# Kernel tuning notes

Hardware: AMD Instinct MI355X
Metric: run time of the kernel (lower is better)

## Reference

```python
import jax, jax.numpy as jnp
import numpy as np

DIM = 1024
HEADS = 32
HEAD_DIM = DIM // HEADS
SR_RATIO = 2
N_RATIO = SR_RATIO * SR_RATIO  # AvgPool1d kernel/stride
BN_EPS = 1e-6


def setup_inputs() -> dict:
    key = jax.random.key(0)
    ks = jax.random.split(key, 10)
    B, N, C = 4, 2048, DIM
    s = C ** -0.5
    return {
        "x": jax.random.normal(ks[0], (B, N, C), dtype=jnp.float32),
        # torch.nn.Linear weights, shape [out, in]; applied as x @ W.T
        "Wq": jax.random.normal(ks[1], (C, C), dtype=jnp.float32) * s,
        "Wk": jax.random.normal(ks[2], (C, C), dtype=jnp.float32) * s,
        "Wv": jax.random.normal(ks[3], (C, C), dtype=jnp.float32) * s,
        "Wp": jax.random.normal(ks[4], (C, C), dtype=jnp.float32) * s,
        "bp": jax.random.normal(ks[5], (C,), dtype=jnp.float32) * 0.01,
        # BatchNorm1d (eval mode) affine + running stats over channel dim C
        "bn_gamma": jnp.ones((C,), dtype=jnp.float32),
        "bn_beta": jnp.zeros((C,), dtype=jnp.float32),
        "bn_mean": jax.random.normal(ks[6], (C,), dtype=jnp.float32) * 0.01,
        "bn_var": jnp.ones((C,), dtype=jnp.float32) + jax.random.uniform(ks[7], (C,), dtype=jnp.float32) * 0.1,
    }


def reference(x, Wq, Wk, Wv, Wp, bp, bn_gamma, bn_beta, bn_mean, bn_var):
    B, N, C = x.shape
    scale = HEAD_DIM ** -0.5
    # Q from full-resolution tokens
    q = (x @ Wq.T).reshape(B, N, HEADS, HEAD_DIM).transpose(0, 2, 1, 3)  # [B,H,N,d]
    # spatial reduction: AvgPool1d(kernel=N_RATIO, stride=N_RATIO) over tokens
    xr = x.reshape(B, N // N_RATIO, N_RATIO, C).mean(axis=2)  # [B,M,C]
    # BatchNorm1d eval: normalize channel dim with running stats
    xr = (xr - bn_mean) * jax.lax.rsqrt(bn_var + BN_EPS) * bn_gamma + bn_beta
    M = xr.shape[1]
    k = (xr @ Wk.T).reshape(B, M, HEADS, HEAD_DIM).transpose(0, 2, 1, 3)  # [B,H,M,d]
    v = (xr @ Wv.T).reshape(B, M, HEADS, HEAD_DIM).transpose(0, 2, 1, 3)  # [B,H,M,d]
    # NOTE: no softmax in the original module — raw scaled scores feed the second matmul
    attn = jnp.einsum("bhnd,bhmd->bhnm", q, k) * scale  # [B,H,N,M]
    out = jnp.einsum("bhnm,bhmd->bhnd", attn, v)        # [B,H,N,d]
    out = out.transpose(0, 2, 1, 3).reshape(B, N, C)
    return out @ Wp.T + bp
```

## Files before the change

### kernel.cpp

```cpp
#include <hip/hip_runtime.h>
#include <stdint.h>

#define DEVFN __device__ __forceinline__

typedef __attribute__((ext_vector_type(8))) short s16x8;
typedef __attribute__((ext_vector_type(4))) float f32x4;

DEVFN float bf2f(uint16_t u) {
  union { uint32_t i; float f; } v; v.i = ((uint32_t)u) << 16; return v.f;
}
DEVFN uint16_t f2bf(float f) {
  union { float f; uint32_t i; } v; v.f = f;
  uint32_t u = v.i;
  return (uint16_t)((u + 0x7FFFu + ((u >> 16) & 1u)) >> 16);
}

DEVFN void gload_lds16(const void* g, void* l) {
  __builtin_amdgcn_global_load_lds(
      (const __attribute__((address_space(1))) uint32_t*)g,
      (__attribute__((address_space(3))) uint32_t*)l, 16, 0, 0);
}

__global__ __launch_bounds__(256)
void prep_kernel(const float* __restrict__ x,
                 const float* __restrict__ bn_g, const float* __restrict__ bn_b,
                 const float* __restrict__ bn_m, const float* __restrict__ bn_v,
                 const float* __restrict__ Wk, const float* __restrict__ Wv,
                 const float* __restrict__ Wp,
                 uint16_t* __restrict__ Xh,
                 uint16_t* __restrict__ XRh,
                 uint16_t* __restrict__ Wkvh,
                 uint16_t* __restrict__ Wph)
{
  const int t = threadIdx.x;
  const int bid = blockIdx.x;
  if (bid < 2048) {
    const int prow = bid;
    const int c0 = t * 4;
    const size_t xbase = (size_t)prow * 4096 + c0;
    float s[4] = {0.f, 0.f, 0.f, 0.f};
#pragma unroll
    for (int r = 0; r < 4; ++r) {
      const float4 w = *(const float4*)(x + xbase + (size_t)r * 1024);
      const float vv[4] = { w.x, w.y, w.z, w.w };
      uint64_t wh = 0;
#pragma unroll
      for (int j = 0; j < 4; ++j) {
        wh |= ((uint64_t)f2bf(vv[j])) << (16 * j);
        s[j] += vv[j];
      }
      *(uint64_t*)(Xh + xbase + (size_t)r * 1024) = wh;
    }
    uint64_t wh = 0;
#pragma unroll
    for (int j = 0; j < 4; ++j) {
      const int c = c0 + j;
      const float y = (s[j] * 0.25f - bn_m[c]) / sqrtf(bn_v[c] + 1e-6f) * bn_g[c] + bn_b[c];
      wh |= ((uint64_t)f2bf(y)) << (16 * j);
    }
    *(uint64_t*)(XRh + (size_t)prow * 1024 + c0) = wh;
  } else {
    const int wb = bid - 2048;
    const int which = wb >> 10;
    const int i = (wb & 1023) * 256 + t;
    const float* src = (which == 0) ? Wk : (which == 1) ? Wv : Wp;
    const float4 v = ((const float4*)src)[i];
    const float vv[4] = { v.x, v.y, v.z, v.w };
    uint64_t wh = 0;
#pragma unroll
    for (int j = 0; j < 4; ++j)
      wh |= ((uint64_t)f2bf(vv[j])) << (16 * j);
    if (which == 2) {
      ((uint64_t*)Wph)[i] = wh;
    } else {
      ((uint64_t*)Wkvh)[(size_t)which * (1024 * 1024 / 4) + i] = wh;
    }
  }
}

template<bool BATCHB, bool AMODA, int EPI, bool KSPLIT2, bool SMALLM>
__global__ __launch_bounds__(256, 2)
void gemm_nt(const uint16_t* __restrict__ A0,
             const uint16_t* __restrict__ B0,
             float* __restrict__ C32, uint16_t* __restrict__ Cb0,
             const float* __restrict__ bias,
             int M, int N, int K, int rows_per_batch)
{
  constexpr int BM = SMALLM ? 64 : 128, BN = 128, BK = 128;
  constexpr int WCN = SMALLM ? 4 : 2;
  constexpr int WNW = BN / WCN;
  constexpr int NREP = WNW / 16;
  constexpr int APASS = SMALLM ? 4 : 8;
  constexpr int BPASS = 8;
  __shared__ uint16_t sA[BM * BK];
  __shared__ uint16_t sB[BN * BK];

  const int t = threadIdx.x;
  const int lane = t & 63;
  const int wave = t >> 6;
  const int wr = wave / WCN, wc = wave % WCN;
  const int fq = lane >> 4, fr = lane & 15;

  const int nwg = gridDim.x;
  const int cpx = nwg >> 3;
  const int orig = blockIdx.x;
  const int swz = (orig & 7) * cpx + (orig >> 3);
  const int nbx = N >> 7;
  const int bm = (swz / nbx) * BM;
  const int bn = (swz % nbx) * BN;

  const uint16_t* Ap = A0;
  const uint16_t* Bp = B0;
  if (BATCHB)
    Bp += (size_t)(bm / rows_per_batch) * (size_t)N * (size_t)K;
  if (KSPLIT2) {
    const size_t half = (size_t)blockIdx.y * M * N;
    if (EPI == 1) Cb0 += half; else C32 += half;
  }

  f32x4 acc[4][NREP];
#pragma unroll
  for (int m = 0; m < 4; ++m)
#pragma unroll
    for (int n = 0; n < NREP; ++n) acc[m][n] = (f32x4)0.0f;

  auto STAGE = [&](int kt) {
#pragma unroll
    for (int i = 0; i < APASS; ++i) {
      const int X = t * 16 + i * 4096;
      const int r = X >> 8;
      const int g = ((X >> 4) & 15) ^ (r & 7);
      const int kcol = (kt << 7) + g * 8;
      const int arow = AMODA ? ((bm + r) & 1023) : (bm + r);
      gload_lds16(Ap + (size_t)arow * K + kcol, (char*)(&sA[0]) + X);
    }
#pragma unroll
    for (int i = 0; i < BPASS; ++i) {
      const int X = t * 16 + i * 4096;
      const int r = X >> 8;
      const int g = ((X >> 4) & 15) ^ (r & 7);
      const int kcol = (kt << 7) + g * 8;
      gload_lds16(Bp + (size_t)(bn + r) * K + kcol, (char*)(&sB[0]) + X);
    }
  };

  const int nkt = K >> (KSPLIT2 ? 8 : 7);
  const int kt0 = KSPLIT2 ? (blockIdx.y * nkt) : 0;
  const int ktend = kt0 + nkt;

  STAGE(kt0);
  for (int kt = kt0; kt < ktend; ++kt) {
    __syncthreads();

    s16x8 av[4][4], bv[4][NREP];
#pragma unroll
    for (int ks = 0; ks < 4; ++ks) {
#pragma unroll
      for (int m = 0; m < 4; ++m) {
        const int ra = wr * 64 + m * 16 + fr;
        const int offA = ra * 256 + ((((ks << 2) + fq) ^ (ra & 7)) << 4);
        av[ks][m] = *(const s16x8*)((const char*)(&sA[0]) + offA);
      }
#pragma unroll
      for (int n = 0; n < NREP; ++n) {
        const int rb = wc * WNW + n * 16 + fr;
        const int offB = rb * 256 + ((((ks << 2) + fq) ^ (rb & 7)) << 4);
        bv[ks][n] = *(const s16x8*)((const char*)(&sB[0]) + offB);
      }
    }

    __syncthreads();
    if (kt + 1 < ktend) STAGE(kt + 1);

#pragma unroll
    for (int ks = 0; ks < 4; ++ks)
#pragma unroll
      for (int m = 0; m < 4; ++m)
#pragma unroll
        for (int n = 0; n < NREP; ++n)
          acc[m][n] = __builtin_amdgcn_mfma_f32_16x16x32_bf16(
              av[ks][m], bv[ks][n], acc[m][n], 0, 0, 0);
  }

#pragma unroll
  for (int m = 0; m < 4; ++m) {
#pragma unroll
    for (int n = 0; n < NREP; ++n) {
#pragma unroll
      for (int j = 0; j < 4; ++j) {
        const int row = bm + wr * 64 + m * 16 + fq * 4 + j;
        const int col = bn + wc * WNW + n * 16 + fr;
        const size_t idx = (size_t)row * N + col;
        float v = acc[m][n][j];
        if constexpr (EPI == 0) {
          C32[idx] = v;
        } else if constexpr (EPI == 1) {
          Cb0[idx] = f2bf(v);
        } else {
          C32[idx] = v + bias[col];
        }
      }
    }
  }
}

__global__ __launch_bounds__(256)
void kv1_kernel(const uint16_t* __restrict__ KVcat, float* __restrict__ part)
{
  const int bid = blockIdx.x;
  const int bh = bid >> 3, ch = bid & 7;
  const int b = bh >> 5, h = bh & 31;
  const int t = threadIdx.x;
  __shared__ float sK[64][32];
  __shared__ float sV[64][32];
  const int f = t >> 3, e0 = (t & 7) * 4;
  const int lr = t >> 2, q = t & 3;
  const size_t rowb = (size_t)(b * 512 + ch * 64 + lr) * 2048 + h * 32 + q * 8;
  const size_t H = (size_t)2048 * 2048;
  const s16x8 k0 = *(const s16x8*)(KVcat + rowb);
  const s16x8 k1 = *(const s16x8*)(KVcat + H + rowb);
  const s16x8 v0 = *(const s16x8*)(KVcat + rowb + 1024);
  const s16x8 v1 = *(const s16x8*)(KVcat + H + rowb + 1024);
#pragma unroll
  for (int j = 0; j < 8; ++j) {
    sK[lr][q * 8 + j] = bf2f((uint16_t)k0[j]) + bf2f((uint16_t)k1[j]);
    sV[lr][q * 8 + j] = bf2f((uint16_t)v0[j]) + bf2f((uint16_t)v1[j]);
  }
  __syncthreads();
  float a0 = 0.f, a1 = 0.f, a2 = 0.f, a3 = 0.f;
#pragma unroll 16
  for (int mm = 0; mm < 64; ++mm) {
    const float kf = sK[mm][f];
    const float4 vv = *(const float4*)&sV[mm][e0];
    a0 += kf * vv.x; a1 += kf * vv.y; a2 += kf * vv.z; a3 += kf * vv.w;
  }
  float* o = part + ((size_t)bid * 32 + f) * 32 + e0;
  o[0] = a0; o[1] = a1; o[2] = a2; o[3] = a3;
}

__global__ __launch_bounds__(256)
void t_kernel(const float* __restrict__ part, const float* __restrict__ Wq,
              uint16_t* __restrict__ Tth)
{
  const int bid = blockIdx.x;
  const int b = bid >> 7, h = (bid >> 2) & 31, cc = bid & 3;
  const int bh = b * 32 + h;
  const int t = threadIdx.x;
  __shared__ float sKV[32][32];
  {
    const int f = t >> 3, e0 = (t & 7) * 4;
    f32x4 a = (f32x4)0.0f;
#pragma unroll
    for (int ch = 0; ch < 8; ++ch)
      a += *(const f32x4*)(part + ((size_t)(bh * 8 + ch) * 32 + f) * 32 + e0);
    a *= 0.17677669529663687f;
    *(f32x4*)&sKV[f][e0] = a;
  }
  __syncthreads();
  const int c = cc * 256 + t;
  f32x4 acc[8];
#pragma unroll
  for (int i = 0; i < 8; ++i) acc[i] = (f32x4)0.0f;
  const float* wqp = Wq + (size_t)(h * 32) * 1024 + c;
#pragma unroll 8
  for (int f = 0; f < 32; ++f) {
    const float wq = wqp[(size_t)f * 1024];
#pragma unroll
    for (int i = 0; i < 8; ++i) {
      const f32x4 kv = *(const f32x4*)&sKV[f][i * 4];
      acc[i] += kv * wq;
    }
  }
  const size_t o = (((size_t)b << 10) + c) * 1024 + h * 32;
#pragma unroll
  for (int i = 0; i < 8; ++i) {
    uint64_t wh = 0;
#pragma unroll
    for (int j = 0; j < 4; ++j)
      wh |= ((uint64_t)f2bf(acc[i][j])) << (16 * j);
    *(uint64_t*)(Tth + o + i * 4) = wh;
  }
}

extern "C" void kernel_launch(void* const* d_in, const int* in_sizes, int n_in,
                              void* d_out, int out_size, void* d_ws, size_t ws_size,
                              hipStream_t stream)
{
  const float* x   = (const float*)d_in[0];
  const float* Wq  = (const float*)d_in[1];
  const float* Wk  = (const float*)d_in[2];
  const float* Wv  = (const float*)d_in[3];
  const float* Wp  = (const float*)d_in[4];
  const float* bp  = (const float*)d_in[5];
  const float* bng = (const float*)d_in[6];
  const float* bnb = (const float*)d_in[7];
  const float* bnm = (const float*)d_in[8];
  const float* bnv = (const float*)d_in[9];
  float* out = (float*)d_out;

  char* ws = (char*)d_ws;
  size_t off = 0;
  auto alloc = [&](size_t bytes) {
    char* p = ws + off;
    off += (bytes + 255) & ~(size_t)255;
    return p;
  };
  uint16_t* Xh   = (uint16_t*)alloc((size_t)8192 * 1024 * 2);
  uint16_t* XRh  = (uint16_t*)alloc((size_t)2048 * 1024 * 2);
  uint16_t* Wkvh = (uint16_t*)alloc((size_t)2048 * 1024 * 2);
  uint16_t* Wph  = (uint16_t*)alloc((size_t)1024 * 1024 * 2);
  uint16_t* KVcat= (uint16_t*)alloc((size_t)2 * 2048 * 2048 * 2);
  uint16_t* Gh   = (uint16_t*)alloc((size_t)4096 * 1024 * 2);
  uint16_t* Tth = KVcat;
  float* KVpart = (float*)Gh;

  prep_kernel<<<5120, 256, 0, stream>>>(x, bng, bnb, bnm, bnv, Wk, Wv, Wp,
                                        Xh, XRh, Wkvh, Wph);
  gemm_nt<false, false, 1, true, false><<<dim3(256, 2), 256, 0, stream>>>(
      XRh, Wkvh, nullptr, KVcat, nullptr,
      2048, 2048, 1024, 1 << 30);
  kv1_kernel<<<1024, 256, 0, stream>>>(KVcat, KVpart);
  t_kernel<<<512, 256, 0, stream>>>(KVpart, Wq, Tth);
  gemm_nt<true, true, 1, false, true><<<512, 256, 0, stream>>>(
      Wph, Tth, nullptr, Gh, nullptr,
      4096, 1024, 1024, 1024);
  gemm_nt<true, false, 2, false, false><<<512, 256, 0, stream>>>(
      Xh, Gh, out, nullptr, bp,
      8192, 1024, 1024, 2048);
}
```

Baseline: 85.47 us.

## Switch GEMM to 32x32x16 MFMA and drop register-prefetch overlap

Replaces the 16x16x32 bf16 MFMA tiling with 32x32x16 MFMA instructions, reorganizing the per-wave accumulators, LDS fragment reads and the epilogue index mapping. The main loop is also restructured: the prior scheme loaded all LDS fragments into registers, then issued the next tile's global->LDS copy before computing. Now each iteration stages, syncs, then reads and computes per k-slice. Larger MFMA tiles cut LDS reads per flop and register pressure. The cost is that global loads no longer overlap with MFMA work.

```diff
diff --git a/kernel.cpp b/kernel.cpp
--- a/kernel.cpp
+++ b/kernel.cpp
@@ -5,6 +5,7 @@
 
 typedef __attribute__((ext_vector_type(8))) short s16x8;
 typedef __attribute__((ext_vector_type(4))) float f32x4;
+typedef __attribute__((ext_vector_type(16))) float f32x16;
 
 DEVFN float bf2f(uint16_t u) {
   union { uint32_t i; float f; } v; v.i = ((uint32_t)u) << 16; return v.f;
@@ -89,7 +90,8 @@
   constexpr int BM = SMALLM ? 64 : 128, BN = 128, BK = 128;
   constexpr int WCN = SMALLM ? 4 : 2;
   constexpr int WNW = BN / WCN;
-  constexpr int NREP = WNW / 16;
+  constexpr int NT = WNW / 32;
+  constexpr int MT = 2;
   constexpr int APASS = SMALLM ? 4 : 8;
   constexpr int BPASS = 8;
   __shared__ uint16_t sA[BM * BK];
@@ -99,7 +101,8 @@
   const int lane = t & 63;
   const int wave = t >> 6;
   const int wr = wave / WCN, wc = wave % WCN;
-  const int fq = lane >> 4, fr = lane & 15;
+  const int l31 = lane & 31;
+  const int hi = lane >> 5;
 
   const int nwg = gridDim.x;
   const int cpx = nwg >> 3;
@@ -118,13 +121,16 @@
     if (EPI == 1) Cb0 += half; else C32 += half;
   }
 
-  f32x4 acc[4][NREP];
-#pragma unroll
-  for (int m = 0; m < 4; ++m)
-#pragma unroll
-    for (int n = 0; n < NREP; ++n) acc[m][n] = (f32x4)0.0f;
-
-  auto STAGE = [&](int kt) {
+  f32x16 acc[MT][NT];
+#pragma unroll
+  for (int ma = 0; ma < MT; ++ma)
+#pragma unroll
+    for (int na = 0; na < NT; ++na) acc[ma][na] = (f32x16)0.0f;
+
+  const int nkt = K >> (KSPLIT2 ? 8 : 7);
+  const int kt0 = KSPLIT2 ? (blockIdx.y * nkt) : 0;
+  for (int kt = kt0; kt < kt0 + nkt; ++kt) {
+    __syncthreads();
 #pragma unroll
     for (int i = 0; i < APASS; ++i) {
       const int X = t * 16 + i * 4096;
@@ -142,56 +148,42 @@
       const int kcol = (kt << 7) + g * 8;
       gload_lds16(Bp + (size_t)(bn + r) * K + kcol, (char*)(&sB[0]) + X);
     }
-  };
-
-  const int nkt = K >> (KSPLIT2 ? 8 : 7);
-  const int kt0 = KSPLIT2 ? (blockIdx.y * nkt) : 0;
-  const int ktend = kt0 + nkt;
-
-  STAGE(kt0);
-  for (int kt = kt0; kt < ktend; ++kt) {
     __syncthreads();
-
-    s16x8 av[4][4], bv[4][NREP];
-#pragma unroll
-    for (int ks = 0; ks < 4; ++ks) {
-#pragma unroll
-      for (int m = 0; m < 4; ++m) {
-        const int ra = wr * 64 + m * 16 + fr;
-        const int offA = ra * 256 + ((((ks << 2) + fq) ^ (ra & 7)) << 4);
-        av[ks][m] = *(const s16x8*)((const char*)(&sA[0]) + offA);
+#pragma unroll
+    for (int ks = 0; ks < 8; ++ks) {
+      const int c = (ks << 1) + hi;
+      s16x8 av[MT], bv[NT];
+#pragma unroll
+      for (int ma = 0; ma < MT; ++ma) {
+        const int ra = wr * 64 + ma * 32 + l31;
+        const int offA = ra * 256 + ((c ^ (ra & 7)) << 4);
+        av[ma] = *(const s16x8*)((const char*)(&sA[0]) + offA);
       }
 #pragma unroll
-      for (int n = 0; n < NREP; ++n) {
-        const int rb = wc * WNW + n * 16 + fr;
-        const int offB = rb * 256 + ((((ks << 2) + fq) ^ (rb & 7)) << 4);
-        bv[ks][n] = *(const s16x8*)((const char*)(&sB[0]) + offB);
+      for (int na = 0; na < NT; ++na) {
+        const int rb = wc * WNW + na * 32 + l31;
+        const int offB = rb * 256 + ((c ^ (rb & 7)) << 4);
+        bv[na] = *(const s16x8*)((const char*)(&sB[0]) + offB);
       }
-    }
-
-    __syncthreads();
-    if (kt + 1 < ktend) STAGE(kt + 1);
-
-#pragma unroll
-    for (int ks = 0; ks < 4; ++ks)
-#pragma unroll
-      for (int m = 0; m < 4; ++m)
-#pragma unroll
-        for (int n = 0; n < NREP; ++n)
-          acc[m][n] = __builtin_amdgcn_mfma_f32_16x16x32_bf16(
-              av[ks][m], bv[ks][n], acc[m][n], 0, 0, 0);
-  }
-
-#pragma unroll
-  for (int m = 0; m < 4; ++m) {
-#pragma unroll
-    for (int n = 0; n < NREP; ++n) {
-#pragma unroll
-      for (int j = 0; j < 4; ++j) {
-        const int row = bm + wr * 64 + m * 16 + fq * 4 + j;
-        const int col = bn + wc * WNW + n * 16 + fr;
+#pragma unroll
+      for (int ma = 0; ma < MT; ++ma)
+#pragma unroll
+        for (int na = 0; na < NT; ++na)
+          acc[ma][na] = __builtin_amdgcn_mfma_f32_32x32x16_bf16(
+              av[ma], bv[na], acc[ma][na], 0, 0, 0);
+    }
+  }
+
+#pragma unroll
+  for (int ma = 0; ma < MT; ++ma) {
+#pragma unroll
+    for (int na = 0; na < NT; ++na) {
+#pragma unroll
+      for (int reg = 0; reg < 16; ++reg) {
+        const int row = bm + wr * 64 + ma * 32 + (reg & 3) + 8 * (reg >> 2) + 4 * hi;
+        const int col = bn + wc * WNW + na * 32 + l31;
         const size_t idx = (size_t)row * N + col;
-        float v = acc[m][n][j];
+        float v = acc[ma][na][reg];
         if constexpr (EPI == 0) {
           C32[idx] = v;
         } else if constexpr (EPI == 1) {
```

Result: slower. 89.76 us (+5.0%).
